# Kernel tuning notes

Hardware: AMD Instinct MI355X
Metric: run time of the kernel (lower is better)

Reference implementation:

```python
import jax, jax.numpy as jnp
import numpy as np

N, E, F_IN, D, EF, L, G = 50000, 800000, 92, 64, 50, 3, 128
EPS = 1e-5


def setup_inputs() -> dict:
    key = jax.random.key(0)
    ks = jax.random.split(key, 16)
    Z = 2 * D + EF  # concat dim for CGConv messages
    inp = {
        "x": jax.random.normal(ks[0], (N, F_IN), dtype=jnp.float32),
        "edge_index": jax.random.randint(ks[1], (2, E), 0, N, dtype=jnp.int32),
        "edge_attr": jax.random.uniform(ks[2], (E, EF), dtype=jnp.float32),
        "batch": jnp.sort(jax.random.randint(ks[3], (N,), 0, G, dtype=jnp.int32)),
        "pre_W": jax.random.normal(ks[4], (F_IN, D), dtype=jnp.float32) * 0.05,
        "pre_b": jnp.zeros((D,), jnp.float32),
        "Wf": jax.random.normal(ks[5], (L, Z, D), dtype=jnp.float32) * 0.05,
        "bf": jnp.zeros((L, D), jnp.float32),
        "Ws": jax.random.normal(ks[6], (L, Z, D), dtype=jnp.float32) * 0.05,
        "bs": jnp.zeros((L, D), jnp.float32),
        "bn_gamma": jnp.ones((L, D), jnp.float32) + 0.1 * jax.random.normal(ks[7], (L, D), dtype=jnp.float32),
        "bn_beta": 0.1 * jax.random.normal(ks[8], (L, D), dtype=jnp.float32),
        "bn_mean": 0.1 * jax.random.normal(ks[9], (L, D), dtype=jnp.float32),
        "bn_var": jax.random.uniform(ks[10], (L, D), dtype=jnp.float32, minval=0.5, maxval=1.5),
        "post_W": jax.random.normal(ks[11], (D, D), dtype=jnp.float32) * 0.05,
        "post_b": jnp.zeros((D,), jnp.float32),
        "out_W": jax.random.normal(ks[12], (D, 1), dtype=jnp.float32) * 0.05,
        "out_b": jnp.zeros((1,), jnp.float32),
    }
    return inp


def reference(x, edge_index, edge_attr, batch, pre_W, pre_b, Wf, bf, Ws, bs,
              bn_gamma, bn_beta, bn_mean, bn_var, post_W, post_b, out_W, out_b):
    src = edge_index[0]  # x_j (source)
    dst = edge_index[1]  # x_i (target, aggregation index)

    # pre FC + relu
    h = jax.nn.relu(x @ pre_W + pre_b)

    # in-degree for mean aggregation
    deg = jax.ops.segment_sum(jnp.ones((E,), h.dtype), dst, num_segments=N)
    deg = jnp.maximum(deg, 1.0)[:, None]

    for l in range(L):
        # CGConv: z_ij = [h_i || h_j || e_ij]
        z = jnp.concatenate([h[dst], h[src], edge_attr], axis=-1)  # [E, 2D+EF]
        m = jax.nn.sigmoid(z @ Wf[l] + bf[l]) * jax.nn.softplus(z @ Ws[l] + bs[l])
        agg = jax.ops.segment_sum(m, dst, num_segments=N) / deg
        h = h + agg  # residual in CGConv
        # BatchNorm1d (eval mode, running stats); dropout is identity in eval
        h = bn_gamma[l] * (h - bn_mean[l]) * jax.lax.rsqrt(bn_var[l] + EPS) + bn_beta[l]

    # early global_mean_pool over graphs
    cnt = jax.ops.segment_sum(jnp.ones((N,), h.dtype), batch, num_segments=G)
    cnt = jnp.maximum(cnt, 1.0)[:, None]
    g = jax.ops.segment_sum(h, batch, num_segments=G) / cnt  # [G, D]

    g = jax.nn.relu(g @ post_W + post_b)
    return g @ out_W + out_b  # [G, 1]
```

## Files before the change

kernel.cpp:

```cpp
#include <hip/hip_runtime.h>
#include <cmath>

#define N_NODES 50000
#define N_EDGES 800000
#define F_IN 92
#define DIM 64
#define EF 50
#define NLAYER 3
#define NGRAPH 128
#define ZROWS 178

__global__ __launch_bounds__(256, 3) void pre_fc(const float* __restrict__ x,
                                                 const float* __restrict__ W,
                                                 const float* __restrict__ b,
                                                 float* __restrict__ h, int N)
{
    const int lane = threadIdx.x & 63;
    const int wid  = blockIdx.x * (blockDim.x >> 6) + (threadIdx.x >> 6);
    const int nw   = gridDim.x * (blockDim.x >> 6);
    float w[F_IN];
#pragma unroll
    for (int k = 0; k < F_IN; ++k) w[k] = W[k * DIM + lane];
    const float bb = b[lane];
#pragma unroll 1
    for (int n = wid; n < N; n += nw) {
        const int nu = __builtin_amdgcn_readfirstlane(n);
        const float* xr = x + (size_t)nu * F_IN;
        float a = bb;
#pragma unroll
        for (int k = 0; k < F_IN; ++k) a = fmaf(xr[k], w[k], a);
        h[(size_t)nu * DIM + lane] = fmaxf(a, 0.f);
    }
}

__global__ __launch_bounds__(256) void deg_cnt(const int* __restrict__ ei, int E,
                                               const int* __restrict__ batch, int N,
                                               float* __restrict__ deg,
                                               float* __restrict__ cnt)
{
    const int i = blockIdx.x * blockDim.x + threadIdx.x;
    const int stride = gridDim.x * blockDim.x;
    for (int e = i; e < E; e += stride) unsafeAtomicAdd(&deg[ei[E + e]], 1.f);
    for (int n = i; n < N; n += stride) unsafeAtomicAdd(&cnt[batch[n]], 1.f);
}

__global__ __launch_bounds__(256, 2) void node_proj(const float* __restrict__ h,
                                                    const float* __restrict__ Wfl,
                                                    const float* __restrict__ Wsl,
                                                    const float* __restrict__ bf,
                                                    const float* __restrict__ bs,
                                                    float* __restrict__ Pd,
                                                    float* __restrict__ Ps, int N)
{
    const int lane = threadIdx.x & 63;
    const int wid  = blockIdx.x * (blockDim.x >> 6) + (threadIdx.x >> 6);
    const int nw   = gridDim.x * (blockDim.x >> 6);
    const int half = wid & 1;
    const float* wfb = Wfl + (half ? DIM * DIM : 0);
    const float* wsb = Wsl + (half ? DIM * DIM : 0);
    float wf[DIM], ws[DIM];
#pragma unroll
    for (int k = 0; k < DIM; ++k) { wf[k] = wfb[k * DIM + lane]; ws[k] = wsb[k * DIM + lane]; }
    const float b0 = half ? 0.f : bf[lane];
    const float b1 = half ? 0.f : bs[lane];
    float* P = half ? Ps : Pd;
#pragma unroll 1
    for (int n = (wid >> 1); n < N; n += (nw >> 1)) {
        const int nu = __builtin_amdgcn_readfirstlane(n);
        const float* hr = h + (size_t)nu * DIM;
        float a0 = b0, a1 = b1;
#pragma unroll
        for (int k = 0; k < DIM; ++k) {
            const float v = hr[k];
            a0 = fmaf(v, wf[k], a0);
            a1 = fmaf(v, ws[k], a1);
        }
        P[(size_t)nu * 128 + lane]      = a0;
        P[(size_t)nu * 128 + 64 + lane] = a1;
    }
}

__global__ __launch_bounds__(256, 3) void edge_gate(const int* __restrict__ ei,
                                                    const float* __restrict__ eattr,
                                                    const float* __restrict__ Pd,
                                                    const float* __restrict__ Ps,
                                                    const float* __restrict__ WfE,
                                                    const float* __restrict__ WsE,
                                                    float* __restrict__ agg, int E)
{
    const int lane = threadIdx.x & 63;
    const int wid  = blockIdx.x * (blockDim.x >> 6) + (threadIdx.x >> 6);
    const int nw   = gridDim.x * (blockDim.x >> 6);
    float wf[EF], ws[EF];
#pragma unroll
    for (int k = 0; k < EF; ++k) { wf[k] = WfE[k * DIM + lane]; ws[k] = WsE[k * DIM + lane]; }
#pragma unroll 1
    for (int e = wid; e < E; e += nw) {
        const int eu = __builtin_amdgcn_readfirstlane(e);
        const int s  = ei[eu];
        const int d  = ei[E + eu];
        const float* pd = Pd + (size_t)d * 128;
        const float* ps = Ps + (size_t)s * 128;
        const float pd0 = pd[lane], pd1 = pd[64 + lane];
        const float ps0 = ps[lane], ps1 = ps[64 + lane];
        const float* ear = eattr + (size_t)eu * EF;
        float accf = 0.f, accs = 0.f;
#pragma unroll
        for (int k = 0; k < EF; ++k) {
            const float v = ear[k];
            accf = fmaf(v, wf[k], accf);
            accs = fmaf(v, ws[k], accs);
        }
        const float zf = accf + pd0 + ps0;
        const float zs = accs + pd1 + ps1;
        const float sig = 1.f / (1.f + __expf(-zf));
        const float sp  = fmaxf(zs, 0.f) + __logf(1.f + __expf(-fabsf(zs)));
        unsafeAtomicAdd(&agg[(size_t)d * DIM + lane], sig * sp);
    }
}

__global__ __launch_bounds__(256) void node_update(float* __restrict__ h,
                                                   const float* __restrict__ agg,
                                                   const float* __restrict__ deg,
                                                   const float* __restrict__ gamma,
                                                   const float* __restrict__ beta,
                                                   const float* __restrict__ mean,
                                                   const float* __restrict__ var, int N)
{
    const int lane = threadIdx.x & 63;
    const float g  = gamma[lane];
    const float bt = beta[lane];
    const float mn = mean[lane];
    const float iv = rsqrtf(var[lane] + 1e-5f);
    const int idx = blockIdx.x * blockDim.x + threadIdx.x;
    const int stride = gridDim.x * blockDim.x;
    const int total = N * DIM;
    for (int i = idx; i < total; i += stride) {
        const int n = i >> 6;
        const float inv = 1.f / fmaxf(deg[n], 1.f);
        const float v = h[i] + agg[i] * inv;
        h[i] = fmaf(g, (v - mn) * iv, bt);
    }
}

__global__ __launch_bounds__(256) void pool_sum(const float* __restrict__ h,
                                                const int* __restrict__ batch,
                                                float* __restrict__ gsum, int N)
{
    const int lane = threadIdx.x & 63;
    const int wid  = blockIdx.x * (blockDim.x >> 6) + (threadIdx.x >> 6);
    const int nw   = gridDim.x * (blockDim.x >> 6);
    for (int n = wid; n < N; n += nw) {
        const int nu = __builtin_amdgcn_readfirstlane(n);
        const int b = batch[nu];
        unsafeAtomicAdd(&gsum[(size_t)b * DIM + lane], h[(size_t)nu * DIM + lane]);
    }
}

__global__ __launch_bounds__(64) void head(const float* __restrict__ gsum,
                                           const float* __restrict__ cnt,
                                           const float* __restrict__ postW,
                                           const float* __restrict__ postb,
                                           const float* __restrict__ outW,
                                           const float* __restrict__ outb,
                                           float* __restrict__ out)
{
    const int gi = blockIdx.x;
    const int lane = threadIdx.x;
    const float inv = 1.f / fmaxf(cnt[gi], 1.f);
    const float gval = gsum[(size_t)gi * DIM + lane] * inv;
    float acc = postb[lane];
#pragma unroll
    for (int k = 0; k < DIM; ++k) acc = fmaf(__shfl(gval, k, 64), postW[k * DIM + lane], acc);
    const float t = fmaxf(acc, 0.f);
    float prod = t * outW[lane];
#pragma unroll
    for (int off = 32; off > 0; off >>= 1) prod += __shfl_down(prod, off, 64);
    if (lane == 0) out[gi] = prod + outb[0];
}

extern "C" void kernel_launch(void* const* d_in, const int* in_sizes, int n_in,
                              void* d_out, int out_size, void* d_ws, size_t ws_size,
                              hipStream_t stream)
{
    const float* x     = (const float*)d_in[0];
    const int*   ei    = (const int*)d_in[1];
    const float* eattr = (const float*)d_in[2];
    const int*   batch = (const int*)d_in[3];
    const float* preW  = (const float*)d_in[4];
    const float* preb  = (const float*)d_in[5];
    const float* Wf    = (const float*)d_in[6];
    const float* bf    = (const float*)d_in[7];
    const float* Ws    = (const float*)d_in[8];
    const float* bs    = (const float*)d_in[9];
    const float* gamma = (const float*)d_in[10];
    const float* beta  = (const float*)d_in[11];
    const float* mean  = (const float*)d_in[12];
    const float* var   = (const float*)d_in[13];
    const float* postW = (const float*)d_in[14];
    const float* postb = (const float*)d_in[15];
    const float* outW  = (const float*)d_in[16];
    const float* outb  = (const float*)d_in[17];
    float* out = (float*)d_out;

    const int N = N_NODES, E = N_EDGES, G = NGRAPH;

    char* p = (char*)d_ws;
    float* h    = (float*)p; p += (size_t)N * DIM * 4;
    float* Pd   = (float*)p; p += (size_t)N * 128 * 4;
    float* Ps   = (float*)p; p += (size_t)N * 128 * 4;
    float* agg  = (float*)p; p += (size_t)N * DIM * 4;
    float* deg  = (float*)p; p += (size_t)N * 4;
    float* gsum = (float*)p; p += (size_t)G * DIM * 4;
    float* cnt  = (float*)p; p += (size_t)G * 4;

    hipMemsetAsync(deg, 0, ((size_t)N + G * DIM + G) * 4, stream);

    pre_fc<<<512, 256, 0, stream>>>(x, preW, preb, h, N);
    deg_cnt<<<512, 256, 0, stream>>>(ei, E, batch, N, deg, cnt);

    for (int l = 0; l < NLAYER; ++l) {
        const float* Wfl = Wf + (size_t)l * ZROWS * DIM;
        const float* Wsl = Ws + (size_t)l * ZROWS * DIM;
        hipMemsetAsync(agg, 0, (size_t)N * DIM * 4, stream);
        node_proj<<<512, 256, 0, stream>>>(h, Wfl, Wsl, bf + l * DIM, bs + l * DIM, Pd, Ps, N);
        edge_gate<<<2048, 256, 0, stream>>>(ei, eattr, Pd, Ps,
                                            Wfl + 2 * DIM * DIM, Wsl + 2 * DIM * DIM, agg, E);
        node_update<<<1024, 256, 0, stream>>>(h, agg, deg, gamma + l * DIM, beta + l * DIM,
                                              mean + l * DIM, var + l * DIM, N);
    }

    pool_sum<<<512, 256, 0, stream>>>(h, batch, gsum, N);
    head<<<G, 64, 0, stream>>>(gsum, cnt, postW, postb, outW, outb, out);
}
```

Baseline: 1.225 ms.

## Process edges and nodes in register blocks, streaming weights instead of caching

The edge gate, node projection and pre-FC kernels now handle several edges or nodes per wavefront (EB=8, NB=4). Each weight element is loaded once per block and reused across those rows, instead of pinning whole weight columns in registers. This lowers register pressure so occupancy can rise (launch bounds go to 4), and it issues more independent gathers per iteration to hide latency. The cost is weight reloads from cache each block. The code also assumes E and N divide evenly by the block sizes, otherwise tail rows are silently dropped.

```diff
diff --git a/kernel.cpp b/kernel.cpp
--- a/kernel.cpp
+++ b/kernel.cpp
@@ -9,8 +9,10 @@
 #define NLAYER 3
 #define NGRAPH 128
 #define ZROWS 178
-
-__global__ __launch_bounds__(256, 3) void pre_fc(const float* __restrict__ x,
+#define EB 8
+#define NB 4
+
+__global__ __launch_bounds__(256, 4) void pre_fc(const float* __restrict__ x,
                                                  const float* __restrict__ W,
                                                  const float* __restrict__ b,
                                                  float* __restrict__ h, int N)
@@ -18,18 +20,24 @@
     const int lane = threadIdx.x & 63;
     const int wid  = blockIdx.x * (blockDim.x >> 6) + (threadIdx.x >> 6);
     const int nw   = gridDim.x * (blockDim.x >> 6);
-    float w[F_IN];
-#pragma unroll
-    for (int k = 0; k < F_IN; ++k) w[k] = W[k * DIM + lane];
     const float bb = b[lane];
+    const int nblk = N / NB;
 #pragma unroll 1
-    for (int n = wid; n < N; n += nw) {
-        const int nu = __builtin_amdgcn_readfirstlane(n);
-        const float* xr = x + (size_t)nu * F_IN;
-        float a = bb;
-#pragma unroll
-        for (int k = 0; k < F_IN; ++k) a = fmaf(xr[k], w[k], a);
-        h[(size_t)nu * DIM + lane] = fmaxf(a, 0.f);
+    for (int blk = wid; blk < nblk; blk += nw) {
+        const int n0 = __builtin_amdgcn_readfirstlane(blk) * NB;
+        const float* xr = x + (size_t)n0 * F_IN;
+        float a[NB];
+#pragma unroll
+        for (int i = 0; i < NB; ++i) a[i] = bb;
+#pragma unroll
+        for (int k = 0; k < F_IN; ++k) {
+            const float wk = W[k * DIM + lane];
+#pragma unroll
+            for (int i = 0; i < NB; ++i) a[i] = fmaf(xr[i * F_IN + k], wk, a[i]);
+        }
+#pragma unroll
+        for (int i = 0; i < NB; ++i)
+            h[(size_t)(n0 + i) * DIM + lane] = fmaxf(a[i], 0.f);
     }
 }
 
@@ -44,7 +52,7 @@
     for (int n = i; n < N; n += stride) unsafeAtomicAdd(&cnt[batch[n]], 1.f);
 }
 
-__global__ __launch_bounds__(256, 2) void node_proj(const float* __restrict__ h,
+__global__ __launch_bounds__(256, 4) void node_proj(const float* __restrict__ h,
                                                     const float* __restrict__ Wfl,
                                                     const float* __restrict__ Wsl,
                                                     const float* __restrict__ bf,
@@ -58,29 +66,37 @@
     const int half = wid & 1;
     const float* wfb = Wfl + (half ? DIM * DIM : 0);
     const float* wsb = Wsl + (half ? DIM * DIM : 0);
-    float wf[DIM], ws[DIM];
-#pragma unroll
-    for (int k = 0; k < DIM; ++k) { wf[k] = wfb[k * DIM + lane]; ws[k] = wsb[k * DIM + lane]; }
     const float b0 = half ? 0.f : bf[lane];
     const float b1 = half ? 0.f : bs[lane];
     float* P = half ? Ps : Pd;
+    const int nblk = N / NB;
 #pragma unroll 1
-    for (int n = (wid >> 1); n < N; n += (nw >> 1)) {
-        const int nu = __builtin_amdgcn_readfirstlane(n);
-        const float* hr = h + (size_t)nu * DIM;
-        float a0 = b0, a1 = b1;
+    for (int blk = (wid >> 1); blk < nblk; blk += (nw >> 1)) {
+        const int n0 = __builtin_amdgcn_readfirstlane(blk) * NB;
+        const float* hr = h + (size_t)n0 * DIM;
+        float a0[NB], a1[NB];
+#pragma unroll
+        for (int i = 0; i < NB; ++i) { a0[i] = b0; a1[i] = b1; }
 #pragma unroll
         for (int k = 0; k < DIM; ++k) {
-            const float v = hr[k];
-            a0 = fmaf(v, wf[k], a0);
-            a1 = fmaf(v, ws[k], a1);
-        }
-        P[(size_t)nu * 128 + lane]      = a0;
-        P[(size_t)nu * 128 + 64 + lane] = a1;
-    }
-}
-
-__global__ __launch_bounds__(256, 3) void edge_gate(const int* __restrict__ ei,
+            const float wfk = wfb[k * DIM + lane];
+            const float wsk = wsb[k * DIM + lane];
+#pragma unroll
+            for (int i = 0; i < NB; ++i) {
+                const float v = hr[i * DIM + k];
+                a0[i] = fmaf(v, wfk, a0[i]);
+                a1[i] = fmaf(v, wsk, a1[i]);
+            }
+        }
+#pragma unroll
+        for (int i = 0; i < NB; ++i) {
+            P[(size_t)(n0 + i) * 128 + lane]      = a0[i];
+            P[(size_t)(n0 + i) * 128 + 64 + lane] = a1[i];
+        }
+    }
+}
+
+__global__ __launch_bounds__(256, 4) void edge_gate(const int* __restrict__ ei,
                                                     const float* __restrict__ eattr,
                                                     const float* __restrict__ Pd,
                                                     const float* __restrict__ Ps,
@@ -91,31 +107,44 @@
     const int lane = threadIdx.x & 63;
     const int wid  = blockIdx.x * (blockDim.x >> 6) + (threadIdx.x >> 6);
     const int nw   = gridDim.x * (blockDim.x >> 6);
-    float wf[EF], ws[EF];
-#pragma unroll
-    for (int k = 0; k < EF; ++k) { wf[k] = WfE[k * DIM + lane]; ws[k] = WsE[k * DIM + lane]; }
+    const int nblk = E / EB;
 #pragma unroll 1
-    for (int e = wid; e < E; e += nw) {
-        const int eu = __builtin_amdgcn_readfirstlane(e);
-        const int s  = ei[eu];
-        const int d  = ei[E + eu];
-        const float* pd = Pd + (size_t)d * 128;
-        const float* ps = Ps + (size_t)s * 128;
-        const float pd0 = pd[lane], pd1 = pd[64 + lane];
-        const float ps0 = ps[lane], ps1 = ps[64 + lane];
-        const float* ear = eattr + (size_t)eu * EF;
-        float accf = 0.f, accs = 0.f;
+    for (int blk = wid; blk < nblk; blk += nw) {
+        const int e0 = __builtin_amdgcn_readfirstlane(blk) * EB;
+        int s[EB], d[EB];
+#pragma unroll
+        for (int i = 0; i < EB; ++i) { s[i] = ei[e0 + i]; d[i] = ei[E + e0 + i]; }
+        float pd0[EB], pd1[EB], ps0[EB], ps1[EB];
+#pragma unroll
+        for (int i = 0; i < EB; ++i) {
+            const float* pd = Pd + (size_t)d[i] * 128;
+            const float* ps = Ps + (size_t)s[i] * 128;
+            pd0[i] = pd[lane]; pd1[i] = pd[64 + lane];
+            ps0[i] = ps[lane]; ps1[i] = ps[64 + lane];
+        }
+        const float* eb = eattr + (size_t)e0 * EF;
+        float accf[EB], accs[EB];
+#pragma unroll
+        for (int i = 0; i < EB; ++i) { accf[i] = 0.f; accs[i] = 0.f; }
 #pragma unroll
         for (int k = 0; k < EF; ++k) {
-            const float v = ear[k];
-            accf = fmaf(v, wf[k], accf);
-            accs = fmaf(v, ws[k], accs);
-        }
-        const float zf = accf + pd0 + ps0;
-        const float zs = accs + pd1 + ps1;
-        const float sig = 1.f / (1.f + __expf(-zf));
-        const float sp  = fmaxf(zs, 0.f) + __logf(1.f + __expf(-fabsf(zs)));
-        unsafeAtomicAdd(&agg[(size_t)d * DIM + lane], sig * sp);
+            const float wfk = WfE[k * DIM + lane];
+            const float wsk = WsE[k * DIM + lane];
+#pragma unroll
+            for (int i = 0; i < EB; ++i) {
+                const float ev = eb[i * EF + k];
+                accf[i] = fmaf(ev, wfk, accf[i]);
+                accs[i] = fmaf(ev, wsk, accs[i]);
+            }
+        }
+#pragma unroll
+        for (int i = 0; i < EB; ++i) {
+            const float zf = accf[i] + pd0[i] + ps0[i];
+            const float zs = accs[i] + pd1[i] + ps1[i];
+            const float sig = 1.f / (1.f + __expf(-zf));
+            const float sp  = fmaxf(zs, 0.f) + __logf(1.f + __expf(-fabsf(zs)));
+            unsafeAtomicAdd(&agg[(size_t)d[i] * DIM + lane], sig * sp);
+        }
     }
 }
 
```

Measured after the change: 2.838 ms. 2.32x slower.

## Tile edge-attribute projection per 64-edge block via LDS staging

Applied to the files above, without the earlier changes.

Replaces the one-edge-per-wave edge kernel with a block that handles 64 edges. The block loads those edges' attributes into padded LDS with coalesced reads. Each thread then computes 32 output columns for one edge, reading weights uniformly across the wave so they can be scalar loads, and writes the results to a transposed LDS tile. A final phase gathers the node projections, applies the gate and does the atomic scatter. The aim is to drop the uncoalesced per-edge attribute loads and the 100 weight registers per lane, at the cost of extra LDS traffic, two barriers, and a grid that assumes E is divisible by 64.

```diff
diff --git a/kernel.cpp b/kernel.cpp
--- a/kernel.cpp
+++ b/kernel.cpp
@@ -80,42 +80,76 @@
     }
 }
 
-__global__ __launch_bounds__(256, 3) void edge_gate(const int* __restrict__ ei,
-                                                    const float* __restrict__ eattr,
-                                                    const float* __restrict__ Pd,
-                                                    const float* __restrict__ Ps,
-                                                    const float* __restrict__ WfE,
-                                                    const float* __restrict__ WsE,
-                                                    float* __restrict__ agg, int E)
-{
-    const int lane = threadIdx.x & 63;
-    const int wid  = blockIdx.x * (blockDim.x >> 6) + (threadIdx.x >> 6);
-    const int nw   = gridDim.x * (blockDim.x >> 6);
-    float wf[EF], ws[EF];
-#pragma unroll
-    for (int k = 0; k < EF; ++k) { wf[k] = WfE[k * DIM + lane]; ws[k] = WsE[k * DIM + lane]; }
-#pragma unroll 1
-    for (int e = wid; e < E; e += nw) {
-        const int eu = __builtin_amdgcn_readfirstlane(e);
-        const int s  = ei[eu];
-        const int d  = ei[E + eu];
-        const float* pd = Pd + (size_t)d * 128;
-        const float* ps = Ps + (size_t)s * 128;
-        const float pd0 = pd[lane], pd1 = pd[64 + lane];
-        const float ps0 = ps[lane], ps1 = ps[64 + lane];
-        const float* ear = eattr + (size_t)eu * EF;
-        float accf = 0.f, accs = 0.f;
-#pragma unroll
+#define EA_PAD 51
+#define TP_PAD 129
+__global__ __launch_bounds__(256) void edge_fused(const int* __restrict__ ei,
+                                                  const float* __restrict__ eattr,
+                                                  const float* __restrict__ Pd,
+                                                  const float* __restrict__ Ps,
+                                                  const float* __restrict__ WfE,
+                                                  const float* __restrict__ WsE,
+                                                  float* __restrict__ agg, int E)
+{
+    __shared__ float ea_lds[64 * EA_PAD];
+    __shared__ float out_lds[64 * TP_PAD];
+
+    const int tid = threadIdx.x;
+    const int e0  = blockIdx.x * 64;
+
+    {
+        const float* src = eattr + (size_t)e0 * EF;
+        for (int idx = tid; idx < 64 * EF; idx += 256) {
+            const int e = idx / EF;
+            const int k = idx - e * EF;
+            ea_lds[e * EA_PAD + k] = src[idx];
+        }
+    }
+    __syncthreads();
+
+    {
+        const int e  = tid & 63;
+        const int wv = __builtin_amdgcn_readfirstlane(threadIdx.x >> 6);
+        const float* Wbase = (wv < 2) ? WfE : WsE;
+        const int c0 = (wv & 1) * 32;
+        const int cb = wv * 32;
+
+        float acc[32];
+#pragma unroll
+        for (int j = 0; j < 32; ++j) acc[j] = 0.f;
+
+        const float* ear = ea_lds + e * EA_PAD;
+#pragma unroll 1
         for (int k = 0; k < EF; ++k) {
-            const float v = ear[k];
-            accf = fmaf(v, wf[k], accf);
-            accs = fmaf(v, ws[k], accs);
-        }
-        const float zf = accf + pd0 + ps0;
-        const float zs = accs + pd1 + ps1;
-        const float sig = 1.f / (1.f + __expf(-zf));
-        const float sp  = fmaxf(zs, 0.f) + __logf(1.f + __expf(-fabsf(zs)));
-        unsafeAtomicAdd(&agg[(size_t)d * DIM + lane], sig * sp);
+            const float eak = ear[k];
+            const float* wr = Wbase + k * DIM + c0;
+#pragma unroll
+            for (int j = 0; j < 32; ++j) acc[j] = fmaf(eak, wr[j], acc[j]);
+        }
+        float* orow = out_lds + e * TP_PAD + cb;
+#pragma unroll
+        for (int j = 0; j < 32; ++j) orow[j] = acc[j];
+    }
+    __syncthreads();
+
+    {
+        const int lane = tid & 63;
+        const int wv   = __builtin_amdgcn_readfirstlane(threadIdx.x >> 6);
+#pragma unroll 1
+        for (int i = 0; i < 16; ++i) {
+            const int el = wv * 16 + i;
+            const int eg = e0 + el;
+            const int s  = ei[eg];
+            const int d  = ei[E + eg];
+            const float pf = out_lds[el * TP_PAD + lane];
+            const float psv = out_lds[el * TP_PAD + 64 + lane];
+            const float* pdr = Pd + (size_t)d * 128;
+            const float* psr = Ps + (size_t)s * 128;
+            const float zf = pf  + pdr[lane]      + psr[lane];
+            const float zs = psv + pdr[64 + lane] + psr[64 + lane];
+            const float sig = 1.f / (1.f + __expf(-zf));
+            const float sp  = fmaxf(zs, 0.f) + __logf(1.f + __expf(-fabsf(zs)));
+            unsafeAtomicAdd(&agg[(size_t)d * DIM + lane], sig * sp);
+        }
     }
 }
 
@@ -224,8 +258,8 @@
         const float* Wsl = Ws + (size_t)l * ZROWS * DIM;
         hipMemsetAsync(agg, 0, (size_t)N * DIM * 4, stream);
         node_proj<<<512, 256, 0, stream>>>(h, Wfl, Wsl, bf + l * DIM, bs + l * DIM, Pd, Ps, N);
-        edge_gate<<<2048, 256, 0, stream>>>(ei, eattr, Pd, Ps,
-                                            Wfl + 2 * DIM * DIM, Wsl + 2 * DIM * DIM, agg, E);
+        edge_fused<<<E / 64, 256, 0, stream>>>(ei, eattr, Pd, Ps,
+                                               Wfl + 2 * DIM * DIM, Wsl + 2 * DIM * DIM, agg, E);
         node_update<<<1024, 256, 0, stream>>>(h, agg, deg, gamma + l * DIM, beta + l * DIM,
                                               mean + l * DIM, var + l * DIM, N);
     }
```

Result: slower. 1.704 ms (+39.1%).
